# Performance work log

Hardware: AMD Instinct MI355X
Metric: run time of the kernel (lower is better)

Reference implementation:

```python
import jax, jax.numpy as jnp
import numpy as np

B, H, W, D = 8, 32, 32, 384      # batch, height, width, channels (=dim)
E, HID, O = 8, 1536, 384         # num_experts, mlp hidden (dim*4), out_dim
TOP_K = 2


def setup_inputs() -> dict:
    key = jax.random.key(0)
    ks = jax.random.split(key, 5)
    x = jax.random.normal(ks[0], (B, H, W, D), dtype=jnp.float32)
    # router (noise_linear unused: eval path, train=False)
    Wg = 0.02 * jax.random.normal(ks[1], (D, E), dtype=jnp.float32)
    bg = jnp.zeros((E,), dtype=jnp.float32)
    # per-expert MLP params stacked along expert axis
    W1 = 0.02 * jax.random.normal(ks[2], (E, D, HID), dtype=jnp.float32)
    b1 = jnp.zeros((E, HID), dtype=jnp.float32)
    W2 = 0.02 * jax.random.normal(ks[3], (E, HID, O), dtype=jnp.float32)
    b2 = jnp.zeros((E, O), dtype=jnp.float32)
    return {"x": x, "Wg": Wg, "bg": bg, "W1": W1, "b1": b1, "W2": W2, "b2": b2}


def reference(x, Wg, bg, W1, b1, W2, b2):
    # --- NoisyTopkRouter (eval: train=False -> no noise branch) ---
    logits = jnp.einsum('bhwd,de->bhwe', x, Wg) + bg            # [B,H,W,E]
    _, top_idx = jax.lax.top_k(logits, TOP_K)                   # [B,H,W,K]
    # mask of selected experts; sparse logits = logits where selected, -inf else
    sel = jnp.sum(jax.nn.one_hot(top_idx, E, dtype=jnp.float32), axis=-2) > 0
    sparse_logits = jnp.where(sel, logits, -jnp.inf)
    gates = jax.nn.softmax(sparse_logits, axis=-1)              # zero on non-top-k

    # --- experts: since gate is exactly 0 off the top-k, the masked
    # gather-MLP-scatter loop equals a gate-weighted sum of all expert MLPs ---
    h = jnp.einsum('bhwd,edf->bhwef', x, W1) + b1               # [B,H,W,E,HID]
    h = jax.nn.gelu(h, approximate=False)                       # torch nn.GELU = exact
    y = jnp.einsum('bhwef,efo->bhweo', h, W2) + b2              # [B,H,W,E,O]
    out = jnp.einsum('bhweo,bhwe->bhwo', y, gates)              # [B,H,W,O]
    return out
```

## Files before the change

### kernel.cpp

```cpp
#include <hip/hip_runtime.h>
#include <cmath>

#define N_TOK 8192
#define DIM   384
#define NEXP  8
#define HID   1536
#define OUTD  384
#define CAP_MT 72
#define CAP_TOK 2304
#define CAP_TB 18

typedef __attribute__((ext_vector_type(8)))  __bf16 bf16x8;
typedef __attribute__((ext_vector_type(16))) float  f32x16;
typedef __attribute__((ext_vector_type(4)))  float  f32x4;
typedef __attribute__((ext_vector_type(8)))  unsigned short u16x8;

__device__ __forceinline__ unsigned short f2bf(float f) {
    unsigned u = __float_as_uint(f);
    u += 0x7FFF + ((u >> 16) & 1);
    return (unsigned short)(u >> 16);
}

__device__ __forceinline__ float bf2f(unsigned short s) {
    return __uint_as_float(((unsigned)s) << 16);
}

__device__ __forceinline__ float gelu_exact(float x) {
    return 0.5f * x * (1.0f + erff(x * 0.70710678118654752f));
}

__device__ __forceinline__ void cp16(const unsigned short* g, unsigned short* l) {
    __builtin_amdgcn_global_load_lds(
        (const __attribute__((address_space(1))) unsigned int*)g,
        (__attribute__((address_space(3))) unsigned int*)l, 16, 0, 0);
}

__global__ void swizzle_kernel(const float* __restrict__ W1, const float* __restrict__ W2,
                               unsigned short* __restrict__ w1s, unsigned short* __restrict__ w2s,
                               int* __restrict__ cnt) {
    if (blockIdx.x == 0 && threadIdx.x < NEXP) cnt[threadIdx.x] = 0;
    int gid = blockIdx.x * blockDim.x + threadIdx.x;
    const int T1 = NEXP * 48 * 24 * 64;
    const int T2 = NEXP * 12 * 96 * 64;
    const float* src; unsigned short* dst; int K, N, NT, KT, g;
    if (gid < T1)           { src = W1; dst = w1s; K = DIM; N = HID;  NT = 48; KT = 24; g = gid; }
    else if (gid < T1 + T2) { src = W2; dst = w2s; K = HID; N = OUTD; NT = 12; KT = 96; g = gid - T1; }
    else return;
    int l  = g & 63;
    int kt = (g >> 6) % KT;
    int nt = ((g >> 6) / KT) % NT;
    int e  = g / (64 * KT * NT);
    const float* s = src + ((size_t)e * K + kt * 16 + (l >> 5) * 8) * N + nt * 32 + (l & 31);
    unsigned short r[8];
    #pragma unroll
    for (int j = 0; j < 8; ++j) r[j] = f2bf(s[(size_t)j * N]);
    *(uint4*)(dst + (size_t)g * 8) = *(uint4*)r;
}

__global__ void router_kernel(const float* __restrict__ x, const float* __restrict__ Wg,
                              const float* __restrict__ bg, int* __restrict__ cnt,
                              int* __restrict__ btok, int* __restrict__ tokmap,
                              float* __restrict__ gmap) {
    __shared__ float WgL[NEXP * DIM];
    __shared__ int lcnt[NEXP];
    __shared__ int lbase[NEXP];
    int tid = threadIdx.x;
    for (int i = tid; i < DIM * NEXP; i += 256) {
        int ch = i >> 3, e = i & 7;
        WgL[e * DIM + ch] = Wg[i];
    }
    if (tid < NEXP) lcnt[tid] = 0;
    __syncthreads();

    int tl  = tid >> 3;
    int seg = tid & 7;
    int t   = blockIdx.x * 32 + tl;

    float lg[NEXP] = {0.f, 0.f, 0.f, 0.f, 0.f, 0.f, 0.f, 0.f};
    const float* xr = x + (size_t)t * DIM;
    #pragma unroll
    for (int d4 = 0; d4 < 12; ++d4) {
        float4 v = *(const float4*)(xr + d4 * 32 + seg * 4);
        #pragma unroll
        for (int e = 0; e < NEXP; ++e) {
            float4 w = *(const float4*)&WgL[e * DIM + d4 * 32 + seg * 4];
            lg[e] += v.x * w.x + v.y * w.y + v.z * w.z + v.w * w.w;
        }
    }
    #pragma unroll
    for (int off = 1; off < 8; off <<= 1)
        #pragma unroll
        for (int e = 0; e < NEXP; ++e)
            lg[e] += __shfl_xor(lg[e], off);

    int p0 = 0, p1 = 0, i0 = 0, i1 = 0;
    float g0 = 0.f, g1 = 0.f;
    if (seg == 0) {
        float v0 = -INFINITY, v1 = -INFINITY;
        #pragma unroll
        for (int e = 0; e < NEXP; ++e) {
            float v = lg[e] + bg[e];
            if (v > v0)      { v1 = v0; i1 = i0; v0 = v; i0 = e; }
            else if (v > v1) { v1 = v;  i1 = e; }
        }
        float e1 = expf(v1 - v0);
        g0 = 1.f / (1.f + e1);
        g1 = e1  / (1.f + e1);
        p0 = atomicAdd(&lcnt[i0], 1);
        p1 = atomicAdd(&lcnt[i1], 1);
    }
    __syncthreads();
    if (tid < NEXP) lbase[tid] = atomicAdd(&cnt[tid], lcnt[tid]);
    __syncthreads();
    if (seg == 0) {
        int o0 = lbase[i0] + p0, o1 = lbase[i1] + p1;
        btok[i0 * N_TOK + o0] = t;
        btok[i1 * N_TOK + o1] = t;
        ((int4*)tokmap)[t] = make_int4(i0, o0, i1, o1);
        ((float2*)gmap)[t] = make_float2(g0, g1);
    }
}

__global__ void gather_kernel(const float* __restrict__ x, const int* __restrict__ cnt,
                              const int* __restrict__ btok, unsigned short* __restrict__ xg) {
    int mt = blockIdx.x, e = blockIdx.y;
    int cntE = cnt[e];
    if (mt * 32 >= cntE) return;
    int tid = threadIdx.x;
    int m = tid & 31, kt0 = tid >> 5;
    int pos = mt * 32 + m;
    int idx = (pos < cntE) ? pos : cntE - 1;
    int tok = btok[e * N_TOK + idx];
    const float* xr = x + (size_t)tok * DIM;
    #pragma unroll
    for (int kk = 0; kk < 3; ++kk) {
        int kt = kt0 + kk * 8;
        #pragma unroll
        for (int kh = 0; kh < 2; ++kh) {
            float4 v0 = *(const float4*)(xr + kt * 16 + kh * 8);
            float4 v1 = *(const float4*)(xr + kt * 16 + kh * 8 + 4);
            unsigned short rr[8];
            rr[0] = f2bf(v0.x); rr[1] = f2bf(v0.y); rr[2] = f2bf(v0.z); rr[3] = f2bf(v0.w);
            rr[4] = f2bf(v1.x); rr[5] = f2bf(v1.y); rr[6] = f2bf(v1.z); rr[7] = f2bf(v1.w);
            *(uint4*)(xg + (size_t)(((e * CAP_MT + mt) * 24 + kt) * 64 + kh * 32 + m) * 8) =
                *(uint4*)rr;
        }
    }
}

__global__ __launch_bounds__(512, 4) void gemm1_kernel(
        const unsigned short* __restrict__ xg, const unsigned short* __restrict__ w1s,
        const float* __restrict__ b1, const int* __restrict__ cnt,
        unsigned short* __restrict__ h) {
    int L = blockIdx.x;
    int e = L & 7;
    int r = L >> 3;
    int nb = r % 12;
    int tb = r / 12;
    int cntE = cnt[e];
    if (tb * 128 >= cntE) return;

    __shared__ unsigned short stg[3][12288];

    int tid = threadIdx.x;
    int wave = tid >> 6, lane = tid & 63;
    int m31 = lane & 31, kh = lane >> 5;
    int wm = wave & 1;
    int wn = wave >> 1;

    f32x16 acc[2];
    acc[0] = (f32x16){0.f,0.f,0.f,0.f,0.f,0.f,0.f,0.f,0.f,0.f,0.f,0.f,0.f,0.f,0.f,0.f};
    acc[1] = acc[0];

    const unsigned short* xa = xg  + ((size_t)(e * CAP_MT + tb * 4) * 24) * 512;
    const unsigned short* wb = w1s + ((size_t)(e * 48 + nb * 4) * 24) * 512;

    const unsigned short* sbase = (wave < 4)
        ? xa + ((size_t)wave * 24) * 512 + lane * 8
        : wb + ((size_t)(wave - 4) * 24) * 512 + lane * 8;
    int tbase = (wave < 4) ? wave * 3 : 12 + (wave - 4) * 3;

    auto issue = [&](int ks) {
        unsigned short* dst = &stg[ks % 3][tbase * 512];
        const unsigned short* sk = sbase + (size_t)ks * 1536;
        #pragma unroll
        for (int q = 0; q < 3; ++q)
            cp16(sk + q * 512, dst + q * 512);
    };
    auto consume = [&](int ks) {
        const unsigned short* bufp = stg[ks % 3];
        #pragma unroll
        for (int kt = 0; kt < 3; ++kt) {
            bf16x8 b  = *(const bf16x8*)&bufp[(12 + wn * 3 + kt) * 512 + lane * 8];
            bf16x8 a0 = *(const bf16x8*)&bufp[((wm * 2 + 0) * 3 + kt) * 512 + lane * 8];
            bf16x8 a1 = *(const bf16x8*)&bufp[((wm * 2 + 1) * 3 + kt) * 512 + lane * 8];
            acc[0] = __builtin_amdgcn_mfma_f32_32x32x16_bf16(a0, b, acc[0], 0, 0, 0);
            acc[1] = __builtin_amdgcn_mfma_f32_32x32x16_bf16(a1, b, acc[1], 0, 0, 0);
        }
    };

    issue(0); issue(1);
    for (int ks = 0; ks < 7; ++ks) {
        asm volatile("s_waitcnt vmcnt(3) lgkmcnt(0)" ::: "memory");
        __builtin_amdgcn_sched_barrier(0);
        __builtin_amdgcn_s_barrier();
        __builtin_amdgcn_sched_barrier(0);
        if (ks + 2 < 8) issue(ks + 2);
        consume(ks);
    }
    asm volatile("s_waitcnt vmcnt(0) lgkmcnt(0)" ::: "memory");
    __builtin_amdgcn_sched_barrier(0);
    __builtin_amdgcn_s_barrier();
    __builtin_amdgcn_sched_barrier(0);
    consume(7);

    __syncthreads();
    char* hw = (char*)stg + wave * 5120;
    float bv = b1[e * HID + nb * 128 + wn * 32 + m31];
    #pragma unroll
    for (int s = 0; s < 2; ++s)
        #pragma unroll
        for (int rr = 0; rr < 16; ++rr) {
            int rowl = s * 32 + (rr & 3) + 8 * (rr >> 2) + 4 * kh;
            *(unsigned short*)(hw + rowl * 80 + m31 * 2) = f2bf(gelu_exact(acc[s][rr] + bv));
        }
    #pragma unroll
    for (int mtl = 0; mtl < 2; ++mtl)
        #pragma unroll
        for (int ktl = 0; ktl < 2; ++ktl) {
            uint4 v = *(const uint4*)(hw + (mtl * 32 + m31) * 80 + (ktl * 16 + kh * 8) * 2);
            int mt = tb * 4 + wm * 2 + mtl;
            int kt = nb * 8 + wn * 2 + ktl;
            *(uint4*)(h + ((size_t)((e * CAP_MT + mt) * 96 + kt)) * 512 + lane * 8) = v;
        }
}

__global__ __launch_bounds__(512, 4) void gemm2_kernel(
        const unsigned short* __restrict__ h, const unsigned short* __restrict__ w2s,
        const int* __restrict__ cnt, unsigned short* __restrict__ yp) {
    int L = blockIdx.x;
    int e = L & 7;
    int r = L >> 3;
    int nb = r % 3;
    int tb = r / 3;
    int cntE = cnt[e];
    if (tb * 128 >= cntE) return;

    __shared__ unsigned short stg[3][12288];

    int tid = threadIdx.x;
    int wave = tid >> 6, lane = tid & 63;
    int m31 = lane & 31, kh = lane >> 5;
    int wm = wave & 1;
    int wn = wave >> 1;

    f32x16 acc[2];
    acc[0] = (f32x16){0.f,0.f,0.f,0.f,0.f,0.f,0.f,0.f,0.f,0.f,0.f,0.f,0.f,0.f,0.f,0.f};
    acc[1] = acc[0];

    const unsigned short* xa = h   + ((size_t)(e * CAP_MT + tb * 4) * 96) * 512;
    const unsigned short* wb = w2s + ((size_t)(e * 12 + nb * 4) * 96) * 512;

    const unsigned short* sbase = (wave < 4)
        ? xa + ((size_t)wave * 96) * 512 + lane * 8
        : wb + ((size_t)(wave - 4) * 96) * 512 + lane * 8;
    int tbase = (wave < 4) ? wave * 3 : 12 + (wave - 4) * 3;

    auto issue = [&](int ks) {
        unsigned short* dst = &stg[ks % 3][tbase * 512];
        const unsigned short* sk = sbase + (size_t)ks * 1536;
        #pragma unroll
        for (int q = 0; q < 3; ++q)
            cp16(sk + q * 512, dst + q * 512);
    };
    auto consume = [&](int ks) {
        const unsigned short* bufp = stg[ks % 3];
        #pragma unroll
        for (int kt = 0; kt < 3; ++kt) {
            bf16x8 b  = *(const bf16x8*)&bufp[(12 + wn * 3 + kt) * 512 + lane * 8];
            bf16x8 a0 = *(const bf16x8*)&bufp[((wm * 2 + 0) * 3 + kt) * 512 + lane * 8];
            bf16x8 a1 = *(const bf16x8*)&bufp[((wm * 2 + 1) * 3 + kt) * 512 + lane * 8];
            acc[0] = __builtin_amdgcn_mfma_f32_32x32x16_bf16(a0, b, acc[0], 0, 0, 0);
            acc[1] = __builtin_amdgcn_mfma_f32_32x32x16_bf16(a1, b, acc[1], 0, 0, 0);
        }
    };

    issue(0); issue(1);
    for (int ks = 0; ks < 31; ++ks) {
        asm volatile("s_waitcnt vmcnt(3) lgkmcnt(0)" ::: "memory");
        __builtin_amdgcn_sched_barrier(0);
        __builtin_amdgcn_s_barrier();
        __builtin_amdgcn_sched_barrier(0);
        if (ks + 2 < 32) issue(ks + 2);
        consume(ks);
    }
    asm volatile("s_waitcnt vmcnt(0) lgkmcnt(0)" ::: "memory");
    __builtin_amdgcn_sched_barrier(0);
    __builtin_amdgcn_s_barrier();
    __builtin_amdgcn_sched_barrier(0);
    consume(31);

    __syncthreads();
    char* hw = (char*)stg + wave * 4096;
    #pragma unroll
    for (int s = 0; s < 2; ++s)
        #pragma unroll
        for (int rr = 0; rr < 16; ++rr) {
            int rowl = s * 32 + (rr & 3) + 8 * (rr >> 2) + 4 * kh;
            *(unsigned short*)(hw + rowl * 64 + m31 * 2) = f2bf(acc[s][rr]);
        }
    #pragma unroll
    for (int it = 0; it < 4; ++it) {
        int rowl = it * 16 + (lane >> 2);
        int cc   = lane & 3;
        uint4 v = *(const uint4*)(hw + rowl * 64 + cc * 16);
        int pos = tb * 128 + wm * 64 + rowl;
        *(uint4*)(yp + (size_t)(e * CAP_TOK + pos) * OUTD + nb * 128 + wn * 32 + cc * 8) = v;
    }
}

__global__ void reduce_kernel(const unsigned short* __restrict__ yp,
                              const int* __restrict__ tokmap, const float* __restrict__ gmap,
                              const float* __restrict__ b2, float* __restrict__ out) {
    int gid = blockIdx.x * 256 + threadIdx.x;
    int t = gid / 48, q = gid - t * 48;
    int4   tm = ((const int4*)tokmap)[t];
    float2 g  = ((const float2*)gmap)[t];
    const unsigned short* p0 = yp + ((size_t)(tm.x * CAP_TOK + tm.y)) * OUTD + q * 8;
    const unsigned short* p1 = yp + ((size_t)(tm.z * CAP_TOK + tm.w)) * OUTD + q * 8;
    u16x8 a = __builtin_nontemporal_load((const u16x8*)p0);
    u16x8 b = __builtin_nontemporal_load((const u16x8*)p1);
    const float* c0 = &b2[tm.x * OUTD + q * 8];
    const float* c1 = &b2[tm.z * OUTD + q * 8];
    f32x4 r0, r1;
    #pragma unroll
    for (int j = 0; j < 4; ++j) {
        r0[j] = g.x * (bf2f(a[j]) + c0[j]) + g.y * (bf2f(b[j]) + c1[j]);
        r1[j] = g.x * (bf2f(a[4 + j]) + c0[4 + j]) + g.y * (bf2f(b[4 + j]) + c1[4 + j]);
    }
    float* op = &out[(size_t)t * OUTD + q * 8];
    __builtin_nontemporal_store(r0, (f32x4*)op);
    __builtin_nontemporal_store(r1, (f32x4*)(op + 4));
}

extern "C" void kernel_launch(void* const* d_in, const int* in_sizes, int n_in,
                              void* d_out, int out_size, void* d_ws, size_t ws_size,
                              hipStream_t stream) {
    const float* x  = (const float*)d_in[0];
    const float* Wg = (const float*)d_in[1];
    const float* bg = (const float*)d_in[2];
    const float* W1 = (const float*)d_in[3];
    const float* b1 = (const float*)d_in[4];
    const float* W2 = (const float*)d_in[5];
    const float* b2 = (const float*)d_in[6];
    float* out = (float*)d_out;

    char* ws = (char*)d_ws;
    int*            cnt    = (int*)ws;
    int*            btok   = (int*)(ws + 1024);
    int*            tokmap = (int*)(ws + 263168);
    float*          gmap   = (float*)(ws + 394240);
    unsigned short* xg     = (unsigned short*)(ws + 459776);
    unsigned short* w1s    = (unsigned short*)(ws + 14615552);
    unsigned short* w2s    = (unsigned short*)(ws + 24052736);
    unsigned short* h      = (unsigned short*)(ws + 33489920);
    unsigned short* yp     = xg;

    hipLaunchKernelGGL(swizzle_kernel, dim3(4608), dim3(256), 0, stream,
                       W1, W2, w1s, w2s, cnt);
    hipLaunchKernelGGL(router_kernel, dim3(N_TOK / 32), dim3(256), 0, stream,
                       x, Wg, bg, cnt, btok, tokmap, gmap);
    hipLaunchKernelGGL(gather_kernel, dim3(CAP_MT, NEXP), dim3(256), 0, stream,
                       x, cnt, btok, xg);
    hipLaunchKernelGGL(gemm1_kernel, dim3(NEXP * 12 * CAP_TB), dim3(512), 0, stream,
                       xg, w1s, b1, cnt, h);
    hipLaunchKernelGGL(gemm2_kernel, dim3(NEXP * 3 * CAP_TB), dim3(512), 0, stream,
                       h, w2s, cnt, yp);
    hipLaunchKernelGGL(reduce_kernel, dim3(N_TOK * 48 / 256), dim3(256), 0, stream,
                       yp, tokmap, gmap, b2, out);
}
```

Baseline: 183.8 us.

## Fuse token gather into gemm1 via indexed loads of bf16 activations

The router kernel now also writes a bf16 copy of x in plain token order. The separate gather kernel is removed, and gemm1's A-operand waves load rows straight from that buffer through the per-expert token index list. This saves one kernel launch and one full pass that read x and wrote a packed, permuted bf16 copy. In exchange, gemm1's A loads become row-indirect 16-byte reads with less contiguity, which may lower load efficiency in the main loop.

```diff
diff --git a/kernel.cpp b/kernel.cpp
--- a/kernel.cpp
+++ b/kernel.cpp
@@ -6,7 +6,6 @@
 #define NEXP  8
 #define HID   1536
 #define OUTD  384
-#define CAP_MT 72
 #define CAP_TOK 2304
 #define CAP_TB 18
 
@@ -60,7 +59,7 @@
 __global__ void router_kernel(const float* __restrict__ x, const float* __restrict__ Wg,
                               const float* __restrict__ bg, int* __restrict__ cnt,
                               int* __restrict__ btok, int* __restrict__ tokmap,
-                              float* __restrict__ gmap) {
+                              float* __restrict__ gmap, unsigned short* __restrict__ xb) {
     __shared__ float WgL[NEXP * DIM];
     __shared__ int lcnt[NEXP];
     __shared__ int lbase[NEXP];
@@ -86,6 +85,8 @@
             float4 w = *(const float4*)&WgL[e * DIM + d4 * 32 + seg * 4];
             lg[e] += v.x * w.x + v.y * w.y + v.z * w.z + v.w * w.w;
         }
+        unsigned short rr[4] = {f2bf(v.x), f2bf(v.y), f2bf(v.z), f2bf(v.w)};
+        *(uint2*)(xb + (size_t)t * DIM + d4 * 32 + seg * 4) = *(uint2*)rr;
     }
     #pragma unroll
     for (int off = 1; off < 8; off <<= 1)
@@ -121,37 +122,10 @@
     }
 }
 
-__global__ void gather_kernel(const float* __restrict__ x, const int* __restrict__ cnt,
-                              const int* __restrict__ btok, unsigned short* __restrict__ xg) {
-    int mt = blockIdx.x, e = blockIdx.y;
-    int cntE = cnt[e];
-    if (mt * 32 >= cntE) return;
-    int tid = threadIdx.x;
-    int m = tid & 31, kt0 = tid >> 5;
-    int pos = mt * 32 + m;
-    int idx = (pos < cntE) ? pos : cntE - 1;
-    int tok = btok[e * N_TOK + idx];
-    const float* xr = x + (size_t)tok * DIM;
-    #pragma unroll
-    for (int kk = 0; kk < 3; ++kk) {
-        int kt = kt0 + kk * 8;
-        #pragma unroll
-        for (int kh = 0; kh < 2; ++kh) {
-            float4 v0 = *(const float4*)(xr + kt * 16 + kh * 8);
-            float4 v1 = *(const float4*)(xr + kt * 16 + kh * 8 + 4);
-            unsigned short rr[8];
-            rr[0] = f2bf(v0.x); rr[1] = f2bf(v0.y); rr[2] = f2bf(v0.z); rr[3] = f2bf(v0.w);
-            rr[4] = f2bf(v1.x); rr[5] = f2bf(v1.y); rr[6] = f2bf(v1.z); rr[7] = f2bf(v1.w);
-            *(uint4*)(xg + (size_t)(((e * CAP_MT + mt) * 24 + kt) * 64 + kh * 32 + m) * 8) =
-                *(uint4*)rr;
-        }
-    }
-}
-
 __global__ __launch_bounds__(512, 4) void gemm1_kernel(
-        const unsigned short* __restrict__ xg, const unsigned short* __restrict__ w1s,
-        const float* __restrict__ b1, const int* __restrict__ cnt,
-        unsigned short* __restrict__ h) {
+        const unsigned short* __restrict__ xb, const unsigned short* __restrict__ w1s,
+        const float* __restrict__ b1, const int* __restrict__ btok,
+        const int* __restrict__ cnt, unsigned short* __restrict__ h) {
     int L = blockIdx.x;
     int e = L & 7;
     int r = L >> 3;
@@ -172,20 +146,28 @@
     acc[0] = (f32x16){0.f,0.f,0.f,0.f,0.f,0.f,0.f,0.f,0.f,0.f,0.f,0.f,0.f,0.f,0.f,0.f};
     acc[1] = acc[0];
 
-    const unsigned short* xa = xg  + ((size_t)(e * CAP_MT + tb * 4) * 24) * 512;
     const unsigned short* wb = w1s + ((size_t)(e * 48 + nb * 4) * 24) * 512;
 
-    const unsigned short* sbase = (wave < 4)
-        ? xa + ((size_t)wave * 24) * 512 + lane * 8
-        : wb + ((size_t)(wave - 4) * 24) * 512 + lane * 8;
+    const unsigned short* sbase;
+    int rstep, qstep;
+    if (wave < 4) {
+        int posA = tb * 128 + wave * 32 + m31;
+        int idxA = (posA < cntE) ? posA : cntE - 1;
+        int tokA = btok[e * N_TOK + idxA];
+        sbase = xb + (size_t)tokA * DIM + kh * 8;
+        rstep = 48;  qstep = 16;
+    } else {
+        sbase = wb + ((size_t)(wave - 4) * 24) * 512 + lane * 8;
+        rstep = 1536; qstep = 512;
+    }
     int tbase = (wave < 4) ? wave * 3 : 12 + (wave - 4) * 3;
 
     auto issue = [&](int ks) {
         unsigned short* dst = &stg[ks % 3][tbase * 512];
-        const unsigned short* sk = sbase + (size_t)ks * 1536;
+        const unsigned short* sk = sbase + (size_t)ks * rstep;
         #pragma unroll
         for (int q = 0; q < 3; ++q)
-            cp16(sk + q * 512, dst + q * 512);
+            cp16(sk + q * qstep, dst + q * 512);
     };
     auto consume = [&](int ks) {
         const unsigned short* bufp = stg[ks % 3];
@@ -231,7 +213,7 @@
             uint4 v = *(const uint4*)(hw + (mtl * 32 + m31) * 80 + (ktl * 16 + kh * 8) * 2);
             int mt = tb * 4 + wm * 2 + mtl;
             int kt = nb * 8 + wn * 2 + ktl;
-            *(uint4*)(h + ((size_t)((e * CAP_MT + mt) * 96 + kt)) * 512 + lane * 8) = v;
+            *(uint4*)(h + ((size_t)((e * 72 + mt) * 96 + kt)) * 512 + lane * 8) = v;
         }
 }
 
@@ -258,7 +240,7 @@
     acc[0] = (f32x16){0.f,0.f,0.f,0.f,0.f,0.f,0.f,0.f,0.f,0.f,0.f,0.f,0.f,0.f,0.f,0.f};
     acc[1] = acc[0];
 
-    const unsigned short* xa = h   + ((size_t)(e * CAP_MT + tb * 4) * 96) * 512;
+    const unsigned short* xa = h   + ((size_t)(e * 72 + tb * 4) * 96) * 512;
     const unsigned short* wb = w2s + ((size_t)(e * 12 + nb * 4) * 96) * 512;
 
     const unsigned short* sbase = (wave < 4)
@@ -360,20 +342,18 @@
     int*            btok   = (int*)(ws + 1024);
     int*            tokmap = (int*)(ws + 263168);
     float*          gmap   = (float*)(ws + 394240);
-    unsigned short* xg     = (unsigned short*)(ws + 459776);
+    unsigned short* xb     = (unsigned short*)(ws + 459776);
     unsigned short* w1s    = (unsigned short*)(ws + 14615552);
     unsigned short* w2s    = (unsigned short*)(ws + 24052736);
     unsigned short* h      = (unsigned short*)(ws + 33489920);
-    unsigned short* yp     = xg;
+    unsigned short* yp     = xb;
 
     hipLaunchKernelGGL(swizzle_kernel, dim3(4608), dim3(256), 0, stream,
                        W1, W2, w1s, w2s, cnt);
     hipLaunchKernelGGL(router_kernel, dim3(N_TOK / 32), dim3(256), 0, stream,
-                       x, Wg, bg, cnt, btok, tokmap, gmap);
-    hipLaunchKernelGGL(gather_kernel, dim3(CAP_MT, NEXP), dim3(256), 0, stream,
-                       x, cnt, btok, xg);
+                       x, Wg, bg, cnt, btok, tokmap, gmap, xb);
     hipLaunchKernelGGL(gemm1_kernel, dim3(NEXP * 12 * CAP_TB), dim3(512), 0, stream,
-                       xg, w1s, b1, cnt, h);
+                       xb, w1s, b1, btok, cnt, h);
     hipLaunchKernelGGL(gemm2_kernel, dim3(NEXP * 3 * CAP_TB), dim3(512), 0, stream,
                        h, w2s, cnt, yp);
     hipLaunchKernelGGL(reduce_kernel, dim3(N_TOK * 48 / 256), dim3(256), 0, stream,
```

Result: no change. 183.5 us (-0.2%).
